# Kernel optimization log

Measured on AMD Instinct MI355X. Metric: run time of the kernel, lower is better.

Reference implementation:

```python
import jax, jax.numpy as jnp
from jax import lax
import numpy as np

DIM = 512      # latent channel dim
K = 1024       # codebook size
KS = 320       # conv kernel size (== stride -> non-overlapping frames)
STRIDE = 320
B, L = 16, 160000  # 10s of 16kHz audio


def setup_inputs() -> dict:
    key = jax.random.key(0)
    ks = jax.random.split(key, 8)
    wav = jax.random.normal(ks[0], (B, 1, L), jnp.float32)
    enc_w = jax.random.normal(ks[1], (DIM, 1, KS), jnp.float32) * 0.05
    enc_b = jnp.zeros((DIM,), jnp.float32)
    codebook = jax.random.normal(ks[2], (K, DIM), jnp.float32)
    lin_w = jax.random.normal(ks[3], (DIM, DIM), jnp.float32) * 0.02
    lin_b = jnp.zeros((DIM,), jnp.float32)
    film_w = jax.random.normal(ks[4], (2 * DIM, DIM), jnp.float32) * 0.02
    film_b = jnp.zeros((2 * DIM,), jnp.float32)
    dec_w = jax.random.normal(ks[5], (DIM, 1, KS), jnp.float32) * 0.05
    dec_b = jnp.zeros((1,), jnp.float32)
    return dict(wav=wav, enc_w=enc_w, enc_b=enc_b, codebook=codebook,
                lin_w=lin_w, lin_b=lin_b, film_w=film_w, film_b=film_b,
                dec_w=dec_w, dec_b=dec_b)


def reference(wav, enc_w, enc_b, codebook, lin_w, lin_b, film_w, film_b, dec_w, dec_b):
    # --- NAC encoder: strided Conv1d, wav [B,1,L] -> emb [B,D,T] ---
    emb = lax.conv_general_dilated(
        wav, enc_w, window_strides=(STRIDE,), padding='VALID',
        dimension_numbers=('NCH', 'OIH', 'NCH')) + enc_b[None, :, None]

    # --- time-averaged embedding for conditioning ---
    time_avg = emb.mean(axis=-1)  # [B, D]

    # --- VQ encode: nearest codebook entry per frame ---
    x = emb.transpose(0, 2, 1)  # [B, T, D]
    # squared L2 distances [B, T, K]
    dist = (x * x).sum(-1, keepdims=True) \
         - 2.0 * jnp.einsum('btd,kd->btk', x, codebook) \
         + (codebook * codebook).sum(-1)
    codes = jnp.argmin(dist, axis=-1)  # [B, T] int

    # --- VQ decode: codebook gather ---
    emb_r = codebook[codes].transpose(0, 2, 1)  # [B, D, T]

    # --- linear on pooled embedding ---
    cond = time_avg @ lin_w.T + lin_b  # [B, D]

    # --- FiLM modulation: gamma * x + beta per channel ---
    gb = cond @ film_w.T + film_b      # [B, 2D]
    gamma, beta = jnp.split(gb, 2, axis=-1)
    modulated = gamma[:, :, None] * emb_r + beta[:, :, None]  # [B, D, T]

    # --- NAC decoder: transposed Conv1d back to waveform [B,1,L] ---
    out = lax.conv_transpose(
        modulated, dec_w, strides=(STRIDE,), padding='VALID',
        dimension_numbers=('NCH', 'IOH', 'NCH')) + dec_b[None, :, None]
    return out
```

## Files before the change

kernel.cpp:

```cpp
#include <hip/hip_runtime.h>

#define FR   8000
#define FRP  8192
#define DD   512
#define CK   1024
#define KSZ  320
#define TT   500
#define NB   16

typedef unsigned int u32;
typedef unsigned short u16;
typedef __attribute__((ext_vector_type(8))) short b8;
typedef __attribute__((ext_vector_type(4))) float f4;

__device__ __forceinline__ float bf2f(u16 h) {
    u32 u = ((u32)h) << 16;
    return __builtin_bit_cast(float, u);
}
__device__ __forceinline__ u16 f2bf(float f) {
    u32 u = __builtin_bit_cast(u32, f);
    u32 r = u + 0x7FFFu + ((u >> 16) & 1u);
    return (u16)(r >> 16);
}

__device__ __forceinline__ void gld16(const u16* g, u16* s) {
    __builtin_amdgcn_global_load_lds(
        (const __attribute__((address_space(1))) u32*)g,
        (__attribute__((address_space(3))) u32*)s, 16, 0, 0);
}

__device__ __forceinline__ f4 mfma(b8 a, b8 b, f4 c) {
    return __builtin_amdgcn_mfma_f32_16x16x32_bf16(a, b, c, 0, 0, 0);
}

__device__ __forceinline__ void split8(float4 a, float4 b, u16* dh, u16* dl) {
    float xs[8] = {a.x, a.y, a.z, a.w, b.x, b.y, b.z, b.w};
    union { u16 u[8]; b8 v; } H, L;
#pragma unroll
    for (int i = 0; i < 8; ++i) {
        u16 h = f2bf(xs[i]);
        H.u[i] = h;
        L.u[i] = f2bf(xs[i] - bf2f(h));
    }
    *(b8*)dh = H.v;
    *(b8*)dl = L.v;
}

__global__ __launch_bounds__(256) void k_prep(const float* __restrict__ enc_w,
                                              u16* __restrict__ ewh, u16* __restrict__ ewl,
                                              const float* __restrict__ cb,
                                              u16* __restrict__ cbh, u16* __restrict__ cbl,
                                              const float* __restrict__ dw,
                                              u16* __restrict__ dwfh, u16* __restrict__ dwfl,
                                              float* __restrict__ cbn,
                                              float* __restrict__ tsum) {
    const int bid = blockIdx.x, tid = threadIdx.x;
    if (bid < 80) {
        int i = (bid * 256 + tid) * 8;
        float4 a = *(const float4*)&enc_w[i];
        float4 b = *(const float4*)&enc_w[i + 4];
        split8(a, b, &ewh[i], &ewl[i]);
    } else if (bid < 336) {
        int i = ((bid - 80) * 256 + tid) * 8;
        float4 a = *(const float4*)&cb[i];
        float4 b = *(const float4*)&cb[i + 4];
        split8(a, b, &cbh[i], &cbl[i]);
    } else if (bid < 368) {
        int c = (bid - 336) * 32 + (tid >> 3);
        int l = tid & 7;
        float s = 0.f;
        for (int j = l * 4; j < DD; j += 32) {
            float4 v = *(const float4*)&cb[c * DD + j];
            s += v.x * v.x + v.y * v.y + v.z * v.z + v.w * v.w;
        }
        s += __shfl_xor(s, 1);
        s += __shfl_xor(s, 2);
        s += __shfl_xor(s, 4);
        if (l == 0) cbn[c] = s;
    } else if (bid < 416) {
        int bid2 = bid - 368;
        int d0 = (bid2 & 7) * 64;
        int sb = bid2 >> 3;
        int s0 = sb * 64;
        if (sb == 5) {
            b8 z = {};
#pragma unroll
            for (int k = 0; k < 2; ++k) {
                int lin = tid * 2 + k;
                int row = 320 + (lin >> 3);
                int col = (lin & 7) * 8;
                *(b8*)&dwfh[(size_t)row * DD + d0 + col] = z;
                *(b8*)&dwfl[(size_t)row * DD + d0 + col] = z;
            }
            return;
        }
        __shared__ float t64[64][68];
        const int u0 = 256 - s0;
#pragma unroll
        for (int p = 0; p < 4; ++p) {
            int row = (tid >> 4) + 16 * p;
            int c4 = (tid & 15) * 4;
            float4 v = *(const float4*)&dw[(size_t)(d0 + row) * KSZ + u0 + c4];
            t64[row][c4] = v.x; t64[row][c4 + 1] = v.y;
            t64[row][c4 + 2] = v.z; t64[row][c4 + 3] = v.w;
        }
        __syncthreads();
        const int i = tid >> 2;
        const int jq = (tid & 3) * 16;
        union { u16 u[8]; b8 v; } H0, L0, H1, L1;
#pragma unroll
        for (int j = 0; j < 8; ++j) {
            float m = t64[jq + j][63 - i];
            u16 h = f2bf(m);
            H0.u[j] = h; L0.u[j] = f2bf(m - bf2f(h));
            float m2 = t64[jq + 8 + j][63 - i];
            u16 h2 = f2bf(m2);
            H1.u[j] = h2; L1.u[j] = f2bf(m2 - bf2f(h2));
        }
        size_t o = (size_t)(s0 + i) * DD + d0 + jq;
        *(b8*)&dwfh[o] = H0.v; *(b8*)&dwfh[o + 8] = H1.v;
        *(b8*)&dwfl[o] = L0.v; *(b8*)&dwfl[o + 8] = L1.v;
    } else {
        float4 z = {0.f, 0.f, 0.f, 0.f};
#pragma unroll
        for (int k = 0; k < 8; ++k)
            *(float4*)&tsum[(tid * 8 + k) * 4] = z;
    }
}

#define PIPELINE(NT, STRIDE)                                                  \
    stg(0, 0);                                                                \
    stg(1, STRIDE);                                                           \
    int cur = 0;                                                              \
    for (int t = 0; t < NT; ++t) {                                            \
        if (t < NT - 1) asm volatile("s_waitcnt vmcnt(8)" ::: "memory");      \
        else            asm volatile("s_waitcnt vmcnt(0)" ::: "memory");      \
        __builtin_amdgcn_s_barrier();                                         \
        asm volatile("" ::: "memory");                                        \
        compute(cur);                                                         \
        asm volatile("" ::: "memory");                                        \
        __builtin_amdgcn_s_barrier();                                         \
        if (t < NT - 2) stg(cur, (t + 2) * STRIDE);                           \
        cur ^= 1;                                                             \
    }

struct AW { float4 x0, x1, y0, y1; };

__global__ __launch_bounds__(256, 2) void k_enc(const float* __restrict__ wav,
                                                const u16* __restrict__ Bhg,
                                                const u16* __restrict__ Blg,
                                                const float* __restrict__ eb,
                                                u16* __restrict__ embh,
                                                u16* __restrict__ embl,
                                                float* __restrict__ tsum) {
    __shared__ __align__(16) u16 Ah[2][4096], Al[2][4096], Bh[2][4096], Bl[2][4096];
    __shared__ float tred[2][128][2];
    const int tid = threadIdx.x;
    const int l = tid & 63, w = tid >> 6, wm = w >> 1, wn = w & 1;
    const int lane16 = l & 15, laneK = l >> 4;
    const int g = blockIdx.x;
    const int xcd = g & 7, slot = g >> 3;
    const int f0 = (xcd * 8 + (slot & 7)) * 128;
    const int d0 = (slot >> 3) * 128;

    const int p0 = w * 128 + l, p1 = p0 + 64;
    const int r0 = p0 >> 2, q0 = (p0 & 3) ^ ((r0 >> 1) & 3);
    const int r1 = p1 >> 2, q1 = (p1 & 3) ^ ((r1 >> 1) & 3);
    const u16* gB0h = Bhg + (size_t)(d0 + r0) * KSZ + q0 * 8;
    const u16* gB1h = Bhg + (size_t)(d0 + r1) * KSZ + q1 * 8;
    const u16* gB0l = Blg + (size_t)(d0 + r0) * KSZ + q0 * 8;
    const u16* gB1l = Blg + (size_t)(d0 + r1) * KSZ + q1 * 8;

    const int pa0 = tid, pa1 = tid + 256;
    const int ra0 = pa0 >> 2, qa0 = (pa0 & 3) ^ ((ra0 >> 1) & 3);
    const int ra1 = pa1 >> 2, qa1 = (pa1 & 3) ^ ((ra1 >> 1) & 3);
    int fa0 = f0 + ra0; if (fa0 > FR - 1) fa0 = FR - 1;
    int fa1 = f0 + ra1; if (fa1 > FR - 1) fa1 = FR - 1;
    const float* wv0 = wav + (size_t)fa0 * KSZ + qa0 * 8;
    const float* wv1 = wav + (size_t)fa1 * KSZ + qa1 * 8;

    int offA[4], offB[4];
#pragma unroll
    for (int i = 0; i < 4; ++i) {
        int ra = wm * 64 + i * 16 + lane16;
        offA[i] = (ra * 4 + (laneK ^ ((ra >> 1) & 3))) * 8;
        int rb = wn * 64 + i * 16 + lane16;
        offB[i] = (rb * 4 + (laneK ^ ((rb >> 1) & 3))) * 8;
    }

    f4 zero = {0.f, 0.f, 0.f, 0.f};
    f4 acc[4][4];
#pragma unroll
    for (int i = 0; i < 4; ++i)
#pragma unroll
        for (int j = 0; j < 4; ++j) acc[i][j] = zero;

    auto loadA = [&](int kt) {
        AW v;
        v.x0 = *(const float4*)(wv0 + kt);
        v.x1 = *(const float4*)(wv0 + kt + 4);
        v.y0 = *(const float4*)(wv1 + kt);
        v.y1 = *(const float4*)(wv1 + kt + 4);
        return v;
    };
    auto writeA = [&](int buf, const AW& v) {
        split8(v.x0, v.x1, Ah[buf] + pa0 * 8, Al[buf] + pa0 * 8);
        split8(v.y0, v.y1, Ah[buf] + pa1 * 8, Al[buf] + pa1 * 8);
    };
    auto stgB = [&](int buf, int kt) {
        gld16(gB0h + kt, Bh[buf] + w * 1024);
        gld16(gB1h + kt, Bh[buf] + w * 1024 + 512);
        gld16(gB0l + kt, Bl[buf] + w * 1024);
        gld16(gB1l + kt, Bl[buf] + w * 1024 + 512);
    };
    auto compute = [&](int buf) {
        b8 ah[4], al[4], bh[4], bl[4];
#pragma unroll
        for (int i = 0; i < 4; ++i) {
            ah[i] = *(const b8*)(Ah[buf] + offA[i]);
            al[i] = *(const b8*)(Al[buf] + offA[i]);
            bh[i] = *(const b8*)(Bh[buf] + offB[i]);
            bl[i] = *(const b8*)(Bl[buf] + offB[i]);
        }
#pragma unroll
        for (int mi = 0; mi < 4; ++mi)
#pragma unroll
            for (int ni = 0; ni < 4; ++ni) {
                acc[mi][ni] = mfma(ah[mi], bh[ni], acc[mi][ni]);
                acc[mi][ni] = mfma(ah[mi], bl[ni], acc[mi][ni]);
                acc[mi][ni] = mfma(al[mi], bh[ni], acc[mi][ni]);
            }
    };

    {
        AW v0 = loadA(0);
        AW v1 = loadA(32);
        stgB(0, 0);
        stgB(1, 32);
        writeA(0, v0);
        writeA(1, v1);
    }
    int cur = 0;
    for (int t = 0; t < 10; ++t) {
        if (t < 9) asm volatile("s_waitcnt vmcnt(4) lgkmcnt(0)" ::: "memory");
        else       asm volatile("s_waitcnt vmcnt(0) lgkmcnt(0)" ::: "memory");
        __builtin_amdgcn_s_barrier();
        asm volatile("" ::: "memory");
        compute(cur);
        asm volatile("" ::: "memory");
        __builtin_amdgcn_s_barrier();
        if (t < 8) {
            AW v = loadA((t + 2) * 32);
            stgB(cur, (t + 2) * 32);
            writeA(cur, v);
        }
        cur ^= 1;
    }

    float ebv[4];
#pragma unroll
    for (int ni = 0; ni < 4; ++ni) ebv[ni] = eb[d0 + wn * 64 + ni * 16 + lane16];

    const int bA = f0 / TT;
    const int fB = min((bA + 1) * TT, f0 + 128);
    float sumA[4] = {}, sumB[4] = {};
#pragma unroll
    for (int mi = 0; mi < 4; ++mi)
#pragma unroll
        for (int q = 0; q < 4; ++q) {
            int f = f0 + wm * 64 + mi * 16 + laneK * 4 + q;
            bool live = f < FR;
            bool sideA = f < fB;
#pragma unroll
            for (int ni = 0; ni < 4; ++ni) {
                int d = d0 + wn * 64 + ni * 16 + lane16;
                float v = acc[mi][ni][q] + ebv[ni];
                u16 h = f2bf(v);
                size_t o = (size_t)f * DD + d;
                embh[o] = h;
                embl[o] = f2bf(v - bf2f(h));
                if (live) { if (sideA) sumA[ni] += v; else sumB[ni] += v; }
            }
        }
#pragma unroll
    for (int m = 16; m <= 32; m <<= 1)
#pragma unroll
        for (int ni = 0; ni < 4; ++ni) {
            sumA[ni] += __shfl_xor(sumA[ni], m);
            sumB[ni] += __shfl_xor(sumB[ni], m);
        }
    if (laneK == 0)
#pragma unroll
        for (int ni = 0; ni < 4; ++ni) {
            tred[wm][wn * 64 + ni * 16 + lane16][0] = sumA[ni];
            tred[wm][wn * 64 + ni * 16 + lane16][1] = sumB[ni];
        }
    __syncthreads();
    if (tid < 128 && bA < NB) {
        float a = tred[0][tid][0] + tred[1][tid][0];
        int d = d0 + tid;
        atomicAdd(&tsum[bA * DD + d], a);
        if (fB < f0 + 128 && bA + 1 < NB) {
            float b = tred[0][tid][1] + tred[1][tid][1];
            atomicAdd(&tsum[(bA + 1) * DD + d], b);
        }
    }
}

__global__ __launch_bounds__(256) void k_cond(const float* __restrict__ tsum,
                                              const float* __restrict__ lw,
                                              const float* __restrict__ lb,
                                              float* __restrict__ cond) {
    __shared__ float stv[NB * DD];
    const float inv = 1.0f / TT;
    for (int i = threadIdx.x * 4; i < NB * DD; i += 1024) {
        float4 v = *(const float4*)&tsum[i];
        v.x *= inv; v.y *= inv; v.z *= inv; v.w *= inv;
        *(float4*)&stv[i] = v;
    }
    __syncthreads();
    const int w = threadIdx.x >> 6, lane = threadIdx.x & 63;
    const int row = blockIdx.x * 4 + w;
    float wv[8];
#pragma unroll
    for (int j = 0; j < 8; ++j) wv[j] = lw[(size_t)row * DD + lane + 64 * j];
    float r[NB];
#pragma unroll
    for (int b = 0; b < NB; ++b) {
        float s = 0.f;
#pragma unroll
        for (int j = 0; j < 8; ++j) s += wv[j] * stv[b * DD + lane + 64 * j];
        r[b] = s;
    }
#pragma unroll
    for (int m = 32; m >= 1; m >>= 1)
#pragma unroll
        for (int b = 0; b < NB; ++b) r[b] += __shfl_xor(r[b], m);
    if (lane < NB) cond[lane * DD + row] = r[lane] + lb[row];
}

__global__ __launch_bounds__(256) void k_film(const float* __restrict__ cond,
                                              const float* __restrict__ fw,
                                              const float* __restrict__ fb,
                                              float* __restrict__ gbv) {
    __shared__ float sc[NB * DD];
    for (int i = threadIdx.x * 4; i < NB * DD; i += 1024)
        *(float4*)&sc[i] = *(const float4*)&cond[i];
    __syncthreads();
    const int w = threadIdx.x >> 6, lane = threadIdx.x & 63;
    const int row = blockIdx.x * 4 + w;
    float wv[8];
#pragma unroll
    for (int j = 0; j < 8; ++j) wv[j] = fw[(size_t)row * DD + lane + 64 * j];
    float r[NB];
#pragma unroll
    for (int b = 0; b < NB; ++b) {
        float s = 0.f;
#pragma unroll
        for (int j = 0; j < 8; ++j) s += wv[j] * sc[b * DD + lane + 64 * j];
        r[b] = s;
    }
#pragma unroll
    for (int m = 32; m >= 1; m >>= 1)
#pragma unroll
        for (int b = 0; b < NB; ++b) r[b] += __shfl_xor(r[b], m);
    if (lane < NB) gbv[lane * 2 * DD + row] = r[lane] + fb[row];
}

__global__ __launch_bounds__(256, 2) void k_dist(const u16* __restrict__ Ahg,
                                                 const u16* __restrict__ Alg,
                                                 const u16* __restrict__ Bhg,
                                                 const u16* __restrict__ Blg,
                                                 const float* __restrict__ cbn,
                                                 float* __restrict__ pmin,
                                                 int* __restrict__ pidx) {
    __shared__ __align__(16) u16 Ah[2][4096], Al[2][4096], Bh[2][4096], Bl[2][4096];
    __shared__ float s_best[128][2];
    __shared__ int s_bidx[128][2];
    const int tid = threadIdx.x;
    const int l = tid & 63, w = tid >> 6, wm = w >> 1, wn = w & 1;
    const int lane16 = l & 15, laneK = l >> 4;
    const int g = blockIdx.x;
    const int xcd = g & 7, slot = g >> 3;
    const int f0 = (xcd * 8 + (slot & 7)) * 128;
    const int cy = slot >> 3;
    const int c0 = cy * 128;

    const int p0 = w * 128 + l, p1 = p0 + 64;
    const int r0 = p0 >> 2, q0 = (p0 & 3) ^ ((r0 >> 1) & 3);
    const int r1 = p1 >> 2, q1 = (p1 & 3) ^ ((r1 >> 1) & 3);
    const u16* gA0h = Ahg + (size_t)(f0 + r0) * DD + q0 * 8;
    const u16* gA1h = Ahg + (size_t)(f0 + r1) * DD + q1 * 8;
    const u16* gA0l = Alg + (size_t)(f0 + r0) * DD + q0 * 8;
    const u16* gA1l = Alg + (size_t)(f0 + r1) * DD + q1 * 8;
    const u16* gB0h = Bhg + (size_t)(c0 + r0) * DD + q0 * 8;
    const u16* gB1h = Bhg + (size_t)(c0 + r1) * DD + q1 * 8;
    const u16* gB0l = Blg + (size_t)(c0 + r0) * DD + q0 * 8;
    const u16* gB1l = Blg + (size_t)(c0 + r1) * DD + q1 * 8;

    int offA[4], offB[4];
#pragma unroll
    for (int i = 0; i < 4; ++i) {
        int ra = wm * 64 + i * 16 + lane16;
        offA[i] = (ra * 4 + (laneK ^ ((ra >> 1) & 3))) * 8;
        int rb = wn * 64 + i * 16 + lane16;
        offB[i] = (rb * 4 + (laneK ^ ((rb >> 1) & 3))) * 8;
    }

    f4 zero = {0.f, 0.f, 0.f, 0.f};
    f4 acc[4][4];
#pragma unroll
    for (int i = 0; i < 4; ++i)
#pragma unroll
        for (int j = 0; j < 4; ++j) acc[i][j] = zero;

    auto stg = [&](int buf, int kt) {
        gld16(gA0h + kt, Ah[buf] + w * 1024);
        gld16(gA1h + kt, Ah[buf] + w * 1024 + 512);
        gld16(gA0l + kt, Al[buf] + w * 1024);
        gld16(gA1l + kt, Al[buf] + w * 1024 + 512);
        gld16(gB0h + kt, Bh[buf] + w * 1024);
        gld16(gB1h + kt, Bh[buf] + w * 1024 + 512);
        gld16(gB0l + kt, Bl[buf] + w * 1024);
        gld16(gB1l + kt, Bl[buf] + w * 1024 + 512);
    };
    auto compute = [&](int buf) {
        b8 ah[4], al[4], bh[4], bl[4];
#pragma unroll
        for (int i = 0; i < 4; ++i) {
            ah[i] = *(const b8*)(Ah[buf] + offA[i]);
            al[i] = *(const b8*)(Al[buf] + offA[i]);
            bh[i] = *(const b8*)(Bh[buf] + offB[i]);
            bl[i] = *(const b8*)(Bl[buf] + offB[i]);
        }
#pragma unroll
        for (int mi = 0; mi < 4; ++mi)
#pragma unroll
            for (int ni = 0; ni < 4; ++ni) {
                acc[mi][ni] = mfma(ah[mi], bh[ni], acc[mi][ni]);
                acc[mi][ni] = mfma(ah[mi], bl[ni], acc[mi][ni]);
                acc[mi][ni] = mfma(al[mi], bh[ni], acc[mi][ni]);
            }
    };

    PIPELINE(16, 32)

    float cbv[4];
    int cidx[4];
#pragma unroll
    for (int ni = 0; ni < 4; ++ni) {
        cidx[ni] = c0 + wn * 64 + ni * 16 + lane16;
        cbv[ni] = cbn[cidx[ni]];
    }
#pragma unroll
    for (int mi = 0; mi < 4; ++mi)
#pragma unroll
        for (int q = 0; q < 4; ++q) {
            float best = 3.4e38f;
            int bi = 0x7fffffff;
#pragma unroll
            for (int ni = 0; ni < 4; ++ni) {
                float s = cbv[ni] - 2.0f * acc[mi][ni][q];
                if (s < best || (s == best && cidx[ni] < bi)) { best = s; bi = cidx[ni]; }
            }
#pragma unroll
            for (int m = 8; m >= 1; m >>= 1) {
                float os = __shfl_xor(best, m);
                int oi = __shfl_xor(bi, m);
                if (os < best || (os == best && oi < bi)) { best = os; bi = oi; }
            }
            if (lane16 == 0) {
                int rl = wm * 64 + mi * 16 + laneK * 4 + q;
                s_best[rl][wn] = best;
                s_bidx[rl][wn] = bi;
            }
        }
    __syncthreads();
    if (tid < 128) {
        float b0 = s_best[tid][0], b1 = s_best[tid][1];
        int i0 = s_bidx[tid][0], i1 = s_bidx[tid][1];
        bool t1 = (b1 < b0) || (b1 == b0 && i1 < i0);
        int f = f0 + tid;
        if (f < FR) {
            pmin[f * 8 + cy] = t1 ? b1 : b0;
            pidx[f * 8 + cy] = t1 ? i1 : i0;
        }
    }
}

struct AV {
    float4 c00, c01, g00, g01, e00, e01;
    float4 c10, c11, g10, g11, e10, e11;
};

__global__ __launch_bounds__(256, 2) void k_dec(const float* __restrict__ pmin,
                                                const int* __restrict__ pidx,
                                                const float* __restrict__ cb,
                                                const float* __restrict__ gbv,
                                                const u16* __restrict__ Bhg,
                                                const u16* __restrict__ Blg,
                                                const float* __restrict__ db,
                                                float* __restrict__ out) {
    __shared__ __align__(16) u16 Ah[2][4096], Al[2][4096], Bh[2][4096], Bl[2][4096];
    __shared__ int codes_lds[128];
    __shared__ int b_lds[128];
    const int tid = threadIdx.x;
    const int l = tid & 63, w = tid >> 6, wm = w >> 1, wn = w & 1;
    const int lane16 = l & 15, laneK = l >> 4;
    const int f0 = blockIdx.y * 128, s0 = blockIdx.x * 128;

    if (tid < 128) {
        int f = f0 + tid;
        int fc = (f < FR) ? f : FR - 1;
        float best = pmin[fc * 8];
        int bi = pidx[fc * 8];
#pragma unroll
        for (int y = 1; y < 8; ++y) {
            float s = pmin[fc * 8 + y];
            if (s < best) { best = s; bi = pidx[fc * 8 + y]; }
        }
        codes_lds[tid] = bi;
        b_lds[tid] = fc / TT;
    }
    __syncthreads();

    const int p0 = w * 128 + l, p1 = p0 + 64;
    const int r0 = p0 >> 2, q0 = (p0 & 3) ^ ((r0 >> 1) & 3);
    const int r1 = p1 >> 2, q1 = (p1 & 3) ^ ((r1 >> 1) & 3);
    const u16* gB0h = Bhg + (size_t)(s0 + r0) * DD + q0 * 8;
    const u16* gB1h = Bhg + (size_t)(s0 + r1) * DD + q1 * 8;
    const u16* gB0l = Blg + (size_t)(s0 + r0) * DD + q0 * 8;
    const u16* gB1l = Blg + (size_t)(s0 + r1) * DD + q1 * 8;

    const int pa0 = tid, pa1 = tid + 256;
    const int ra0 = pa0 >> 2, qa0 = (pa0 & 3) ^ ((ra0 >> 1) & 3);
    const int ra1 = pa1 >> 2, qa1 = (pa1 & 3) ^ ((ra1 >> 1) & 3);
    const float* cp0 = cb + (size_t)codes_lds[ra0] * DD + qa0 * 8;
    const float* cp1 = cb + (size_t)codes_lds[ra1] * DD + qa1 * 8;
    const float* gp0 = gbv + b_lds[ra0] * 2 * DD + qa0 * 8;
    const float* gp1 = gbv + b_lds[ra1] * 2 * DD + qa1 * 8;

    int offA[4], offB[4];
#pragma unroll
    for (int i = 0; i < 4; ++i) {
        int ra = wm * 64 + i * 16 + lane16;
        offA[i] = (ra * 4 + (laneK ^ ((ra >> 1) & 3))) * 8;
        int rb = wn * 64 + i * 16 + lane16;
        offB[i] = (rb * 4 + (laneK ^ ((rb >> 1) & 3))) * 8;
    }

    f4 zero = {0.f, 0.f, 0.f, 0.f};
    f4 acc[4][4];
#pragma unroll
    for (int i = 0; i < 4; ++i)
#pragma unroll
        for (int j = 0; j < 4; ++j) acc[i][j] = zero;

    auto stgB = [&](int buf, int kt) {
        gld16(gB0h + kt, Bh[buf] + w * 1024);
        gld16(gB1h + kt, Bh[buf] + w * 1024 + 512);
        gld16(gB0l + kt, Bl[buf] + w * 1024);
        gld16(gB1l + kt, Bl[buf] + w * 1024 + 512);
    };
    auto loadA = [&](int kt) {
        AV v;
        v.c00 = *(const float4*)(cp0 + kt);
        v.c01 = *(const float4*)(cp0 + kt + 4);
        v.g00 = *(const float4*)(gp0 + kt);
        v.g01 = *(const float4*)(gp0 + kt + 4);
        v.e00 = *(const float4*)(gp0 + DD + kt);
        v.e01 = *(const float4*)(gp0 + DD + kt + 4);
        v.c10 = *(const float4*)(cp1 + kt);
        v.c11 = *(const float4*)(cp1 + kt + 4);
        v.g10 = *(const float4*)(gp1 + kt);
        v.g11 = *(const float4*)(gp1 + kt + 4);
        v.e10 = *(const float4*)(gp1 + DD + kt);
        v.e11 = *(const float4*)(gp1 + DD + kt + 4);
        return v;
    };
    auto writeA = [&](int buf, const AV& v) {
        float4 m00, m01, m10, m11;
        m00.x = v.g00.x * v.c00.x + v.e00.x; m00.y = v.g00.y * v.c00.y + v.e00.y;
        m00.z = v.g00.z * v.c00.z + v.e00.z; m00.w = v.g00.w * v.c00.w + v.e00.w;
        m01.x = v.g01.x * v.c01.x + v.e01.x; m01.y = v.g01.y * v.c01.y + v.e01.y;
        m01.z = v.g01.z * v.c01.z + v.e01.z; m01.w = v.g01.w * v.c01.w + v.e01.w;
        m10.x = v.g10.x * v.c10.x + v.e10.x; m10.y = v.g10.y * v.c10.y + v.e10.y;
        m10.z = v.g10.z * v.c10.z + v.e10.z; m10.w = v.g10.w * v.c10.w + v.e10.w;
        m11.x = v.g11.x * v.c11.x + v.e11.x; m11.y = v.g11.y * v.c11.y + v.e11.y;
        m11.z = v.g11.z * v.c11.z + v.e11.z; m11.w = v.g11.w * v.c11.w + v.e11.w;
        split8(m00, m01, Ah[buf] + pa0 * 8, Al[buf] + pa0 * 8);
        split8(m10, m11, Ah[buf] + pa1 * 8, Al[buf] + pa1 * 8);
    };
    auto compute = [&](int buf) {
        b8 ah[4], al[4], bh[4], bl[4];
#pragma unroll
        for (int i = 0; i < 4; ++i) {
            ah[i] = *(const b8*)(Ah[buf] + offA[i]);
            al[i] = *(const b8*)(Al[buf] + offA[i]);
            bh[i] = *(const b8*)(Bh[buf] + offB[i]);
            bl[i] = *(const b8*)(Bl[buf] + offB[i]);
        }
#pragma unroll
        for (int mi = 0; mi < 4; ++mi)
#pragma unroll
            for (int ni = 0; ni < 4; ++ni) {
                acc[mi][ni] = mfma(ah[mi], bh[ni], acc[mi][ni]);
                acc[mi][ni] = mfma(ah[mi], bl[ni], acc[mi][ni]);
                acc[mi][ni] = mfma(al[mi], bh[ni], acc[mi][ni]);
            }
    };

    {
        AV v0 = loadA(0);
        AV v1 = loadA(32);
        stgB(0, 0);
        stgB(1, 32);
        writeA(0, v0);
        writeA(1, v1);
    }
    int cur = 0;
    for (int t = 0; t < 16; ++t) {
        if (t < 15) asm volatile("s_waitcnt vmcnt(4) lgkmcnt(0)" ::: "memory");
        else        asm volatile("s_waitcnt vmcnt(0) lgkmcnt(0)" ::: "memory");
        __builtin_amdgcn_s_barrier();
        asm volatile("" ::: "memory");
        compute(cur);
        asm volatile("" ::: "memory");
        __builtin_amdgcn_s_barrier();
        if (t < 14) {
            AV v = loadA((t + 2) * 32);
            stgB(cur, (t + 2) * 32);
            writeA(cur, v);
        }
        cur ^= 1;
    }

    const float d0v = db[0];
#pragma unroll
    for (int mi = 0; mi < 4; ++mi)
#pragma unroll
        for (int q = 0; q < 4; ++q) {
            int f = f0 + wm * 64 + mi * 16 + laneK * 4 + q;
            if (f < FR) {
#pragma unroll
                for (int ni = 0; ni < 4; ++ni) {
                    int s = s0 + wn * 64 + ni * 16 + lane16;
                    if (s < KSZ) out[(size_t)f * KSZ + s] = acc[mi][ni][q] + d0v;
                }
            }
        }
}

extern "C" void kernel_launch(void* const* d_in, const int* in_sizes, int n_in,
                              void* d_out, int out_size, void* d_ws, size_t ws_size,
                              hipStream_t stream) {
    const float* wav    = (const float*)d_in[0];
    const float* enc_w  = (const float*)d_in[1];
    const float* enc_b  = (const float*)d_in[2];
    const float* cb     = (const float*)d_in[3];
    const float* lin_w  = (const float*)d_in[4];
    const float* lin_b  = (const float*)d_in[5];
    const float* film_w = (const float*)d_in[6];
    const float* film_b = (const float*)d_in[7];
    const float* dec_w  = (const float*)d_in[8];
    const float* dec_b  = (const float*)d_in[9];
    float* out = (float*)d_out;

    char* p = (char*)d_ws;
    u16* embh = (u16*)p;                 p += (size_t)FRP * DD * 2;
    u16* embl = (u16*)p;                 p += (size_t)FRP * DD * 2;
    u16* ewh  = (u16*)p;                 p += (size_t)DD * KSZ * 2;
    u16* ewl  = (u16*)p;                 p += (size_t)DD * KSZ * 2;
    u16* cbh  = (u16*)p;                 p += (size_t)CK * DD * 2;
    u16* cbl  = (u16*)p;                 p += (size_t)CK * DD * 2;
    u16* dwfh = (u16*)p;                 p += (size_t)384 * DD * 2;
    u16* dwfl = (u16*)p;                 p += (size_t)384 * DD * 2;
    float* cbn  = (float*)p;             p += CK * 4;
    float* tsum = (float*)p;             p += NB * DD * 4;
    float* cond = (float*)p;             p += NB * DD * 4;
    float* gbv  = (float*)p;             p += NB * 2 * DD * 4;
    float* pmin = (float*)p;             p += FR * 8 * 4;
    int*   pidx = (int*)p;               p += FR * 8 * 4;

    k_prep<<<dim3(417), 256, 0, stream>>>(enc_w, ewh, ewl, cb, cbh, cbl,
                                          dec_w, dwfh, dwfl, cbn, tsum);
    k_enc<<<dim3(256), 256, 0, stream>>>(wav, ewh, ewl, enc_b, embh, embl, tsum);
    k_cond<<<dim3(128), 256, 0, stream>>>(tsum, lin_w, lin_b, cond);
    k_film<<<dim3(256), 256, 0, stream>>>(cond, film_w, film_b, gbv);
    k_dist<<<dim3(512), 256, 0, stream>>>(embh, embl, cbh, cbl, cbn, pmin, pidx);
    k_dec<<<dim3(3, 63), 256, 0, stream>>>(pmin, pidx, cb, gbv, dwfh, dwfl, dec_b, out);
}
```

Baseline: 172.2 us.

## Use 512-thread blocks for enc/dist, smaller 64x64 tiles for dec, MFMA priority

k_enc and k_dist now run with 8 waves per 128x128 tile, each wave owning a 64x32 sub-tile, so every thread stages fewer global loads and holds fewer accumulators. k_dec moves to 64x64 tiles on a 5x125 grid that exactly covers the 8000x320 output, which removes the bounds checks and padded waste. s_setprio raises wave priority around the MFMA bursts, and k_dist is launched before the small cond/film kernels. The aim is more resident waves to hide latency and better CU utilisation, paid for with more LDS fragment reloads per MFMA and a 4-way cross-wave argmin reduction.

```diff
diff --git a/kernel.cpp b/kernel.cpp
--- a/kernel.cpp
+++ b/kernel.cpp
@@ -128,25 +128,7 @@
     }
 }
 
-#define PIPELINE(NT, STRIDE)                                                  \
-    stg(0, 0);                                                                \
-    stg(1, STRIDE);                                                           \
-    int cur = 0;                                                              \
-    for (int t = 0; t < NT; ++t) {                                            \
-        if (t < NT - 1) asm volatile("s_waitcnt vmcnt(8)" ::: "memory");      \
-        else            asm volatile("s_waitcnt vmcnt(0)" ::: "memory");      \
-        __builtin_amdgcn_s_barrier();                                         \
-        asm volatile("" ::: "memory");                                        \
-        compute(cur);                                                         \
-        asm volatile("" ::: "memory");                                        \
-        __builtin_amdgcn_s_barrier();                                         \
-        if (t < NT - 2) stg(cur, (t + 2) * STRIDE);                           \
-        cur ^= 1;                                                             \
-    }
-
-struct AW { float4 x0, x1, y0, y1; };
-
-__global__ __launch_bounds__(256, 2) void k_enc(const float* __restrict__ wav,
+__global__ __launch_bounds__(512, 4) void k_enc(const float* __restrict__ wav,
                                                 const u16* __restrict__ Bhg,
                                                 const u16* __restrict__ Blg,
                                                 const float* __restrict__ eb,
@@ -156,80 +138,75 @@
     __shared__ __align__(16) u16 Ah[2][4096], Al[2][4096], Bh[2][4096], Bl[2][4096];
     __shared__ float tred[2][128][2];
     const int tid = threadIdx.x;
-    const int l = tid & 63, w = tid >> 6, wm = w >> 1, wn = w & 1;
+    const int l = tid & 63, w = tid >> 6, wm = w >> 2, wn = w & 3;
     const int lane16 = l & 15, laneK = l >> 4;
     const int g = blockIdx.x;
     const int xcd = g & 7, slot = g >> 3;
     const int f0 = (xcd * 8 + (slot & 7)) * 128;
     const int d0 = (slot >> 3) * 128;
 
-    const int p0 = w * 128 + l, p1 = p0 + 64;
-    const int r0 = p0 >> 2, q0 = (p0 & 3) ^ ((r0 >> 1) & 3);
-    const int r1 = p1 >> 2, q1 = (p1 & 3) ^ ((r1 >> 1) & 3);
-    const u16* gB0h = Bhg + (size_t)(d0 + r0) * KSZ + q0 * 8;
-    const u16* gB1h = Bhg + (size_t)(d0 + r1) * KSZ + q1 * 8;
-    const u16* gB0l = Blg + (size_t)(d0 + r0) * KSZ + q0 * 8;
-    const u16* gB1l = Blg + (size_t)(d0 + r1) * KSZ + q1 * 8;
-
-    const int pa0 = tid, pa1 = tid + 256;
-    const int ra0 = pa0 >> 2, qa0 = (pa0 & 3) ^ ((ra0 >> 1) & 3);
-    const int ra1 = pa1 >> 2, qa1 = (pa1 & 3) ^ ((ra1 >> 1) & 3);
-    int fa0 = f0 + ra0; if (fa0 > FR - 1) fa0 = FR - 1;
-    int fa1 = f0 + ra1; if (fa1 > FR - 1) fa1 = FR - 1;
-    const float* wv0 = wav + (size_t)fa0 * KSZ + qa0 * 8;
-    const float* wv1 = wav + (size_t)fa1 * KSZ + qa1 * 8;
-
-    int offA[4], offB[4];
+    const int sr = tid >> 2;
+    const int sq = (tid & 3) ^ ((sr >> 1) & 3);
+    int fa = f0 + sr; if (fa > FR - 1) fa = FR - 1;
+    const float* wv = wav + (size_t)fa * KSZ + sq * 8;
+    const u16* gBh = Bhg + (size_t)(d0 + sr) * KSZ + sq * 8;
+    const u16* gBl = Blg + (size_t)(d0 + sr) * KSZ + sq * 8;
+
+    int offA[4], offB[2];
 #pragma unroll
     for (int i = 0; i < 4; ++i) {
         int ra = wm * 64 + i * 16 + lane16;
         offA[i] = (ra * 4 + (laneK ^ ((ra >> 1) & 3))) * 8;
-        int rb = wn * 64 + i * 16 + lane16;
+    }
+#pragma unroll
+    for (int i = 0; i < 2; ++i) {
+        int rb = wn * 32 + i * 16 + lane16;
         offB[i] = (rb * 4 + (laneK ^ ((rb >> 1) & 3))) * 8;
     }
 
     f4 zero = {0.f, 0.f, 0.f, 0.f};
-    f4 acc[4][4];
+    f4 acc[4][2];
 #pragma unroll
     for (int i = 0; i < 4; ++i)
 #pragma unroll
-        for (int j = 0; j < 4; ++j) acc[i][j] = zero;
-
+        for (int j = 0; j < 2; ++j) acc[i][j] = zero;
+
+    struct AW { float4 x0, x1; };
     auto loadA = [&](int kt) {
         AW v;
-        v.x0 = *(const float4*)(wv0 + kt);
-        v.x1 = *(const float4*)(wv0 + kt + 4);
-        v.y0 = *(const float4*)(wv1 + kt);
-        v.y1 = *(const float4*)(wv1 + kt + 4);
+        v.x0 = *(const float4*)(wv + kt);
+        v.x1 = *(const float4*)(wv + kt + 4);
         return v;
     };
     auto writeA = [&](int buf, const AW& v) {
-        split8(v.x0, v.x1, Ah[buf] + pa0 * 8, Al[buf] + pa0 * 8);
-        split8(v.y0, v.y1, Ah[buf] + pa1 * 8, Al[buf] + pa1 * 8);
+        split8(v.x0, v.x1, Ah[buf] + tid * 8, Al[buf] + tid * 8);
     };
     auto stgB = [&](int buf, int kt) {
-        gld16(gB0h + kt, Bh[buf] + w * 1024);
-        gld16(gB1h + kt, Bh[buf] + w * 1024 + 512);
-        gld16(gB0l + kt, Bl[buf] + w * 1024);
-        gld16(gB1l + kt, Bl[buf] + w * 1024 + 512);
+        gld16(gBh + kt, Bh[buf] + w * 512);
+        gld16(gBl + kt, Bl[buf] + w * 512);
     };
     auto compute = [&](int buf) {
-        b8 ah[4], al[4], bh[4], bl[4];
+        b8 ah[4], al[4], bh[2], bl[2];
 #pragma unroll
         for (int i = 0; i < 4; ++i) {
             ah[i] = *(const b8*)(Ah[buf] + offA[i]);
             al[i] = *(const b8*)(Al[buf] + offA[i]);
+        }
+#pragma unroll
+        for (int i = 0; i < 2; ++i) {
             bh[i] = *(const b8*)(Bh[buf] + offB[i]);
             bl[i] = *(const b8*)(Bl[buf] + offB[i]);
         }
+        __builtin_amdgcn_s_setprio(1);
 #pragma unroll
         for (int mi = 0; mi < 4; ++mi)
 #pragma unroll
-            for (int ni = 0; ni < 4; ++ni) {
+            for (int ni = 0; ni < 2; ++ni) {
                 acc[mi][ni] = mfma(ah[mi], bh[ni], acc[mi][ni]);
                 acc[mi][ni] = mfma(ah[mi], bl[ni], acc[mi][ni]);
                 acc[mi][ni] = mfma(al[mi], bh[ni], acc[mi][ni]);
             }
+        __builtin_amdgcn_s_setprio(0);
     };
 
     {
@@ -242,7 +219,7 @@
     }
     int cur = 0;
     for (int t = 0; t < 10; ++t) {
-        if (t < 9) asm volatile("s_waitcnt vmcnt(4) lgkmcnt(0)" ::: "memory");
+        if (t < 9) asm volatile("s_waitcnt vmcnt(2) lgkmcnt(0)" ::: "memory");
         else       asm volatile("s_waitcnt vmcnt(0) lgkmcnt(0)" ::: "memory");
         __builtin_amdgcn_s_barrier();
         asm volatile("" ::: "memory");
@@ -257,13 +234,13 @@
         cur ^= 1;
     }
 
-    float ebv[4];
-#pragma unroll
-    for (int ni = 0; ni < 4; ++ni) ebv[ni] = eb[d0 + wn * 64 + ni * 16 + lane16];
+    float ebv[2];
+#pragma unroll
+    for (int ni = 0; ni < 2; ++ni) ebv[ni] = eb[d0 + wn * 32 + ni * 16 + lane16];
 
     const int bA = f0 / TT;
     const int fB = min((bA + 1) * TT, f0 + 128);
-    float sumA[4] = {}, sumB[4] = {};
+    float sumA[2] = {}, sumB[2] = {};
 #pragma unroll
     for (int mi = 0; mi < 4; ++mi)
 #pragma unroll
@@ -272,8 +249,8 @@
             bool live = f < FR;
             bool sideA = f < fB;
 #pragma unroll
-            for (int ni = 0; ni < 4; ++ni) {
-                int d = d0 + wn * 64 + ni * 16 + lane16;
+            for (int ni = 0; ni < 2; ++ni) {
+                int d = d0 + wn * 32 + ni * 16 + lane16;
                 float v = acc[mi][ni][q] + ebv[ni];
                 u16 h = f2bf(v);
                 size_t o = (size_t)f * DD + d;
@@ -285,15 +262,15 @@
 #pragma unroll
     for (int m = 16; m <= 32; m <<= 1)
 #pragma unroll
-        for (int ni = 0; ni < 4; ++ni) {
+        for (int ni = 0; ni < 2; ++ni) {
             sumA[ni] += __shfl_xor(sumA[ni], m);
             sumB[ni] += __shfl_xor(sumB[ni], m);
         }
     if (laneK == 0)
 #pragma unroll
-        for (int ni = 0; ni < 4; ++ni) {
-            tred[wm][wn * 64 + ni * 16 + lane16][0] = sumA[ni];
-            tred[wm][wn * 64 + ni * 16 + lane16][1] = sumB[ni];
+        for (int ni = 0; ni < 2; ++ni) {
+            tred[wm][wn * 32 + ni * 16 + lane16][0] = sumA[ni];
+            tred[wm][wn * 32 + ni * 16 + lane16][1] = sumB[ni];
         }
     __syncthreads();
     if (tid < 128 && bA < NB) {
@@ -367,7 +344,7 @@
     if (lane < NB) gbv[lane * 2 * DD + row] = r[lane] + fb[row];
 }
 
-__global__ __launch_bounds__(256, 2) void k_dist(const u16* __restrict__ Ahg,
+__global__ __launch_bounds__(512, 4) void k_dist(const u16* __restrict__ Ahg,
                                                  const u16* __restrict__ Alg,
                                                  const u16* __restrict__ Bhg,
                                                  const u16* __restrict__ Blg,
@@ -375,81 +352,93 @@
                                                  float* __restrict__ pmin,
                                                  int* __restrict__ pidx) {
     __shared__ __align__(16) u16 Ah[2][4096], Al[2][4096], Bh[2][4096], Bl[2][4096];
-    __shared__ float s_best[128][2];
-    __shared__ int s_bidx[128][2];
+    __shared__ float s_best[128][4];
+    __shared__ int s_bidx[128][4];
     const int tid = threadIdx.x;
-    const int l = tid & 63, w = tid >> 6, wm = w >> 1, wn = w & 1;
+    const int l = tid & 63, w = tid >> 6, wm = w >> 2, wn = w & 3;
     const int lane16 = l & 15, laneK = l >> 4;
     const int g = blockIdx.x;
     const int xcd = g & 7, slot = g >> 3;
-    const int f0 = (xcd * 8 + (slot & 7)) * 128;
+    const int fbase = (xcd * 8 + (slot & 7)) * 128;
     const int cy = slot >> 3;
     const int c0 = cy * 128;
 
-    const int p0 = w * 128 + l, p1 = p0 + 64;
-    const int r0 = p0 >> 2, q0 = (p0 & 3) ^ ((r0 >> 1) & 3);
-    const int r1 = p1 >> 2, q1 = (p1 & 3) ^ ((r1 >> 1) & 3);
-    const u16* gA0h = Ahg + (size_t)(f0 + r0) * DD + q0 * 8;
-    const u16* gA1h = Ahg + (size_t)(f0 + r1) * DD + q1 * 8;
-    const u16* gA0l = Alg + (size_t)(f0 + r0) * DD + q0 * 8;
-    const u16* gA1l = Alg + (size_t)(f0 + r1) * DD + q1 * 8;
-    const u16* gB0h = Bhg + (size_t)(c0 + r0) * DD + q0 * 8;
-    const u16* gB1h = Bhg + (size_t)(c0 + r1) * DD + q1 * 8;
-    const u16* gB0l = Blg + (size_t)(c0 + r0) * DD + q0 * 8;
-    const u16* gB1l = Blg + (size_t)(c0 + r1) * DD + q1 * 8;
-
-    int offA[4], offB[4];
+    const int sr = tid >> 2;
+    const int sq = (tid & 3) ^ ((sr >> 1) & 3);
+    const u16* gAh = Ahg + (size_t)(fbase + sr) * DD + sq * 8;
+    const u16* gAl = Alg + (size_t)(fbase + sr) * DD + sq * 8;
+    const u16* gBh = Bhg + (size_t)(c0 + sr) * DD + sq * 8;
+    const u16* gBl = Blg + (size_t)(c0 + sr) * DD + sq * 8;
+
+    int offA[4], offB[2];
 #pragma unroll
     for (int i = 0; i < 4; ++i) {
         int ra = wm * 64 + i * 16 + lane16;
         offA[i] = (ra * 4 + (laneK ^ ((ra >> 1) & 3))) * 8;
-        int rb = wn * 64 + i * 16 + lane16;
+    }
+#pragma unroll
+    for (int i = 0; i < 2; ++i) {
+        int rb = wn * 32 + i * 16 + lane16;
         offB[i] = (rb * 4 + (laneK ^ ((rb >> 1) & 3))) * 8;
     }
 
     f4 zero = {0.f, 0.f, 0.f, 0.f};
-    f4 acc[4][4];
+    f4 acc[4][2];
 #pragma unroll
     for (int i = 0; i < 4; ++i)
 #pragma unroll
-        for (int j = 0; j < 4; ++j) acc[i][j] = zero;
+        for (int j = 0; j < 2; ++j) acc[i][j] = zero;
 
     auto stg = [&](int buf, int kt) {
-        gld16(gA0h + kt, Ah[buf] + w * 1024);
-        gld16(gA1h + kt, Ah[buf] + w * 1024 + 512);
-        gld16(gA0l + kt, Al[buf] + w * 1024);
-        gld16(gA1l + kt, Al[buf] + w * 1024 + 512);
-        gld16(gB0h + kt, Bh[buf] + w * 1024);
-        gld16(gB1h + kt, Bh[buf] + w * 1024 + 512);
-        gld16(gB0l + kt, Bl[buf] + w * 1024);
-        gld16(gB1l + kt, Bl[buf] + w * 1024 + 512);
+        gld16(gAh + kt, Ah[buf] + w * 512);
+        gld16(gAl + kt, Al[buf] + w * 512);
+        gld16(gBh + kt, Bh[buf] + w * 512);
+        gld16(gBl + kt, Bl[buf] + w * 512);
     };
     auto compute = [&](int buf) {
-        b8 ah[4], al[4], bh[4], bl[4];
+        b8 ah[4], al[4], bh[2], bl[2];
 #pragma unroll
         for (int i = 0; i < 4; ++i) {
             ah[i] = *(const b8*)(Ah[buf] + offA[i]);
             al[i] = *(const b8*)(Al[buf] + offA[i]);
+        }
+#pragma unroll
+        for (int i = 0; i < 2; ++i) {
             bh[i] = *(const b8*)(Bh[buf] + offB[i]);
             bl[i] = *(const b8*)(Bl[buf] + offB[i]);
         }
+        __builtin_amdgcn_s_setprio(1);
 #pragma unroll
         for (int mi = 0; mi < 4; ++mi)
 #pragma unroll
-            for (int ni = 0; ni < 4; ++ni) {
+            for (int ni = 0; ni < 2; ++ni) {
                 acc[mi][ni] = mfma(ah[mi], bh[ni], acc[mi][ni]);
                 acc[mi][ni] = mfma(ah[mi], bl[ni], acc[mi][ni]);
                 acc[mi][ni] = mfma(al[mi], bh[ni], acc[mi][ni]);
             }
-    };
-
-    PIPELINE(16, 32)
-
-    float cbv[4];
-    int cidx[4];
-#pragma unroll
-    for (int ni = 0; ni < 4; ++ni) {
-        cidx[ni] = c0 + wn * 64 + ni * 16 + lane16;
+        __builtin_amdgcn_s_setprio(0);
+    };
+
+    stg(0, 0);
+    stg(1, 32);
+    int cur = 0;
+    for (int t = 0; t < 16; ++t) {
+        if (t < 15) asm volatile("s_waitcnt vmcnt(4)" ::: "memory");
+        else        asm volatile("s_waitcnt vmcnt(0)" ::: "memory");
+        __builtin_amdgcn_s_barrier();
+        asm volatile("" ::: "memory");
+        compute(cur);
+        asm volatile("" ::: "memory");
+        __builtin_amdgcn_s_barrier();
+        if (t < 14) stg(cur, (t + 2) * 32);
+        cur ^= 1;
+    }
+
+    float cbv[2];
+    int cidx[2];
+#pragma unroll
+    for (int ni = 0; ni < 2; ++ni) {
+        cidx[ni] = c0 + wn * 32 + ni * 16 + lane16;
         cbv[ni] = cbn[cidx[ni]];
     }
 #pragma unroll
@@ -459,7 +448,7 @@
             float best = 3.4e38f;
             int bi = 0x7fffffff;
 #pragma unroll
-            for (int ni = 0; ni < 4; ++ni) {
+            for (int ni = 0; ni < 2; ++ni) {
                 float s = cbv[ni] - 2.0f * acc[mi][ni][q];
                 if (s < best || (s == best && cidx[ni] < bi)) { best = s; bi = cidx[ni]; }
             }
@@ -477,23 +466,23 @@
         }
     __syncthreads();
     if (tid < 128) {
-        float b0 = s_best[tid][0], b1 = s_best[tid][1];
-        int i0 = s_bidx[tid][0], i1 = s_bidx[tid][1];
-        bool t1 = (b1 < b0) || (b1 == b0 && i1 < i0);
-        int f = f0 + tid;
+        float best = s_best[tid][0];
+        int bi = s_bidx[tid][0];
+#pragma unroll
+        for (int y = 1; y < 4; ++y) {
+            float s = s_best[tid][y];
+            int ii = s_bidx[tid][y];
+            if (s < best || (s == best && ii < bi)) { best = s; bi = ii; }
+        }
+        int f = fbase + tid;
         if (f < FR) {
-            pmin[f * 8 + cy] = t1 ? b1 : b0;
-            pidx[f * 8 + cy] = t1 ? i1 : i0;
-        }
-    }
-}
-
-struct AV {
-    float4 c00, c01, g00, g01, e00, e01;
-    float4 c10, c11, g10, g11, e10, e11;
-};
-
-__global__ __launch_bounds__(256, 2) void k_dec(const float* __restrict__ pmin,
+            pmin[f * 8 + cy] = best;
+            pidx[f * 8 + cy] = bi;
+        }
+    }
+}
+
+__global__ __launch_bounds__(256, 4) void k_dec(const float* __restrict__ pmin,
                                                 const int* __restrict__ pidx,
                                                 const float* __restrict__ cb,
                                                 const float* __restrict__ gbv,
@@ -501,17 +490,16 @@
                                                 const u16* __restrict__ Blg,
                                                 const float* __restrict__ db,
                                                 float* __restrict__ out) {
-    __shared__ __align__(16) u16 Ah[2][4096], Al[2][4096], Bh[2][4096], Bl[2][4096];
-    __shared__ int codes_lds[128];
-    __shared__ int b_lds[128];
+    __shared__ __align__(16) u16 Ah[2][2048], Al[2][2048], Bh[2][2048], Bl[2][2048];
+    __shared__ int codes_lds[64];
+    __shared__ int b_lds[64];
     const int tid = threadIdx.x;
     const int l = tid & 63, w = tid >> 6, wm = w >> 1, wn = w & 1;
     const int lane16 = l & 15, laneK = l >> 4;
-    const int f0 = blockIdx.y * 128, s0 = blockIdx.x * 128;
-
-    if (tid < 128) {
-        int f = f0 + tid;
-        int fc = (f < FR) ? f : FR - 1;
+    const int f0 = blockIdx.y * 64, s0 = blockIdx.x * 64;
+
+    if (tid < 64) {
+        int fc = f0 + tid;
         float best = pmin[fc * 8];
         int bi = pidx[fc * 8];
 #pragma unroll
@@ -524,90 +512,72 @@
     }
     __syncthreads();
 
-    const int p0 = w * 128 + l, p1 = p0 + 64;
-    const int r0 = p0 >> 2, q0 = (p0 & 3) ^ ((r0 >> 1) & 3);
-    const int r1 = p1 >> 2, q1 = (p1 & 3) ^ ((r1 >> 1) & 3);
-    const u16* gB0h = Bhg + (size_t)(s0 + r0) * DD + q0 * 8;
-    const u16* gB1h = Bhg + (size_t)(s0 + r1) * DD + q1 * 8;
-    const u16* gB0l = Blg + (size_t)(s0 + r0) * DD + q0 * 8;
-    const u16* gB1l = Blg + (size_t)(s0 + r1) * DD + q1 * 8;
-
-    const int pa0 = tid, pa1 = tid + 256;
-    const int ra0 = pa0 >> 2, qa0 = (pa0 & 3) ^ ((ra0 >> 1) & 3);
-    const int ra1 = pa1 >> 2, qa1 = (pa1 & 3) ^ ((ra1 >> 1) & 3);
-    const float* cp0 = cb + (size_t)codes_lds[ra0] * DD + qa0 * 8;
-    const float* cp1 = cb + (size_t)codes_lds[ra1] * DD + qa1 * 8;
-    const float* gp0 = gbv + b_lds[ra0] * 2 * DD + qa0 * 8;
-    const float* gp1 = gbv + b_lds[ra1] * 2 * DD + qa1 * 8;
-
-    int offA[4], offB[4];
-#pragma unroll
-    for (int i = 0; i < 4; ++i) {
-        int ra = wm * 64 + i * 16 + lane16;
+    const int sr = tid >> 2;
+    const int sq = (tid & 3) ^ ((sr >> 1) & 3);
+    const float* cp = cb + (size_t)codes_lds[sr] * DD + sq * 8;
+    const float* gp = gbv + b_lds[sr] * 2 * DD + sq * 8;
+    const float* ep = gp + DD;
+    const u16* gBh = Bhg + (size_t)(s0 + sr) * DD + sq * 8;
+    const u16* gBl = Blg + (size_t)(s0 + sr) * DD + sq * 8;
+
+    int offA[2], offB[2];
+#pragma unroll
+    for (int i = 0; i < 2; ++i) {
+        int ra = wm * 32 + i * 16 + lane16;
         offA[i] = (ra * 4 + (laneK ^ ((ra >> 1) & 3))) * 8;
-        int rb = wn * 64 + i * 16 + lane16;
+        int rb = wn * 32 + i * 16 + lane16;
         offB[i] = (rb * 4 + (laneK ^ ((rb >> 1) & 3))) * 8;
     }
 
     f4 zero = {0.f, 0.f, 0.f, 0.f};
-    f4 acc[4][4];
-#pragma unroll
-    for (int i = 0; i < 4; ++i)
-#pragma unroll
-        for (int j = 0; j < 4; ++j) acc[i][j] = zero;
-
-    auto stgB = [&](int buf, int kt) {
-        gld16(gB0h + kt, Bh[buf] + w * 1024);
-        gld16(gB1h + kt, Bh[buf] + w * 1024 + 512);
-        gld16(gB0l + kt, Bl[buf] + w * 1024);
-        gld16(gB1l + kt, Bl[buf] + w * 1024 + 512);
-    };
+    f4 acc[2][2];
+#pragma unroll
+    for (int i = 0; i < 2; ++i)
+#pragma unroll
+        for (int j = 0; j < 2; ++j) acc[i][j] = zero;
+
+    struct AV { float4 c0, c1, g0, g1, e0, e1; };
     auto loadA = [&](int kt) {
         AV v;
-        v.c00 = *(const float4*)(cp0 + kt);
-        v.c01 = *(const float4*)(cp0 + kt + 4);
-        v.g00 = *(const float4*)(gp0 + kt);
-        v.g01 = *(const float4*)(gp0 + kt + 4);
-        v.e00 = *(const float4*)(gp0 + DD + kt);
-        v.e01 = *(const float4*)(gp0 + DD + kt + 4);
-        v.c10 = *(const float4*)(cp1 + kt);
-        v.c11 = *(const float4*)(cp1 + kt + 4);
-        v.g10 = *(const float4*)(gp1 + kt);
-        v.g11 = *(const float4*)(gp1 + kt + 4);
-        v.e10 = *(const float4*)(gp1 + DD + kt);
-        v.e11 = *(const float4*)(gp1 + DD + kt + 4);
+        v.c0 = *(const float4*)(cp + kt);
+        v.c1 = *(const float4*)(cp + kt + 4);
+        v.g0 = *(const float4*)(gp + kt);
+        v.g1 = *(const float4*)(gp + kt + 4);
+        v.e0 = *(const float4*)(ep + kt);
+        v.e1 = *(const float4*)(ep + kt + 4);
         return v;
     };
     auto writeA = [&](int buf, const AV& v) {
-        float4 m00, m01, m10, m11;
-        m00.x = v.g00.x * v.c00.x + v.e00.x; m00.y = v.g00.y * v.c00.y + v.e00.y;
-        m00.z = v.g00.z * v.c00.z + v.e00.z; m00.w = v.g00.w * v.c00.w + v.e00.w;
-        m01.x = v.g01.x * v.c01.x + v.e01.x; m01.y = v.g01.y * v.c01.y + v.e01.y;
-        m01.z = v.g01.z * v.c01.z + v.e01.z; m01.w = v.g01.w * v.c01.w + v.e01.w;
-        m10.x = v.g10.x * v.c10.x + v.e10.x; m10.y = v.g10.y * v.c10.y + v.e10.y;
-        m10.z = v.g10.z * v.c10.z + v.e10.z; m10.w = v.g10.w * v.c10.w + v.e10.w;
-        m11.x = v.g11.x * v.c11.x + v.e11.x; m11.y = v.g11.y * v.c11.y + v.e11.y;
-        m11.z = v.g11.z * v.c11.z + v.e11.z; m11.w = v.g11.w * v.c11.w + v.e11.w;
-        split8(m00, m01, Ah[buf] + pa0 * 8, Al[buf] + pa0 * 8);
-        split8(m10, m11, Ah[buf] + pa1 * 8, Al[buf] + pa1 * 8);
+        float4 m0, m1;
+        m0.x = v.g0.x * v.c0.x + v.e0.x; m0.y = v.g0.y * v.c0.y + v.e0.y;
+        m0.z = v.g0.z * v.c0.z + v.e0.z; m0.w = v.g0.w * v.c0.w + v.e0.w;
+        m1.x = v.g1.x * v.c1.x + v.e1.x; m1.y = v.g1.y * v.c1.y + v.e1.y;
+        m1.z = v.g1.z * v.c1.z + v.e1.z; m1.w = v.g1.w * v.c1.w + v.e1.w;
+        split8(m0, m1, Ah[buf] + tid * 8, Al[buf] + tid * 8);
+    };
+    auto stgB = [&](int buf, int kt) {
+        gld16(gBh + kt, Bh[buf] + w * 512);
+        gld16(gBl + kt, Bl[buf] + w * 512);
     };
     auto compute = [&](int buf) {
-        b8 ah[4], al[4], bh[4], bl[4];
-#pragma unroll
-        for (int i = 0; i < 4; ++i) {
+        b8 ah[2], al[2], bh[2], bl[2];
+#pragma unroll
+        for (int i = 0; i < 2; ++i) {
             ah[i] = *(const b8*)(Ah[buf] + offA[i]);
             al[i] = *(const b8*)(Al[buf] + offA[i]);
             bh[i] = *(const b8*)(Bh[buf] + offB[i]);
             bl[i] = *(const b8*)(Bl[buf] + offB[i]);
         }
-#pragma unroll
-        for (int mi = 0; mi < 4; ++mi)
-#pragma unroll
-            for (int ni = 0; ni < 4; ++ni) {
+        __builtin_amdgcn_s_setprio(1);
+#pragma unroll
+        for (int mi = 0; mi < 2; ++mi)
+#pragma unroll
+            for (int ni = 0; ni < 2; ++ni) {
                 acc[mi][ni] = mfma(ah[mi], bh[ni], acc[mi][ni]);
                 acc[mi][ni] = mfma(ah[mi], bl[ni], acc[mi][ni]);
                 acc[mi][ni] = mfma(al[mi], bh[ni], acc[mi][ni]);
             }
+        __builtin_amdgcn_s_setprio(0);
     };
 
     {
@@ -620,7 +590,7 @@
     }
     int cur = 0;
     for (int t = 0; t < 16; ++t) {
-        if (t < 15) asm volatile("s_waitcnt vmcnt(4) lgkmcnt(0)" ::: "memory");
+        if (t < 15) asm volatile("s_waitcnt vmcnt(2) lgkmcnt(0)" ::: "memory");
         else        asm volatile("s_waitcnt vmcnt(0) lgkmcnt(0)" ::: "memory");
         __builtin_amdgcn_s_barrier();
         asm volatile("" ::: "memory");
@@ -637,16 +607,14 @@
 
     const float d0v = db[0];
 #pragma unroll
-    for (int mi = 0; mi < 4; ++mi)
+    for (int mi = 0; mi < 2; ++mi)
 #pragma unroll
         for (int q = 0; q < 4; ++q) {
-            int f = f0 + wm * 64 + mi * 16 + laneK * 4 + q;
-            if (f < FR) {
-#pragma unroll
-                for (int ni = 0; ni < 4; ++ni) {
-                    int s = s0 + wn * 64 + ni * 16 + lane16;
-                    if (s < KSZ) out[(size_t)f * KSZ + s] = acc[mi][ni][q] + d0v;
-                }
+            int f = f0 + wm * 32 + mi * 16 + laneK * 4 + q;
+#pragma unroll
+            for (int ni = 0; ni < 2; ++ni) {
+                int s = s0 + wn * 32 + ni * 16 + lane16;
+                out[(size_t)f * KSZ + s] = acc[mi][ni][q] + d0v;
             }
         }
 }
@@ -684,9 +652,9 @@
 
     k_prep<<<dim3(417), 256, 0, stream>>>(enc_w, ewh, ewl, cb, cbh, cbl,
                                           dec_w, dwfh, dwfl, cbn, tsum);
-    k_enc<<<dim3(256), 256, 0, stream>>>(wav, ewh, ewl, enc_b, embh, embl, tsum);
+    k_enc<<<dim3(256), 512, 0, stream>>>(wav, ewh, ewl, enc_b, embh, embl, tsum);
+    k_dist<<<dim3(512), 512, 0, stream>>>(embh, embl, cbh, cbl, cbn, pmin, pidx);
     k_cond<<<dim3(128), 256, 0, stream>>>(tsum, lin_w, lin_b, cond);
     k_film<<<dim3(256), 256, 0, stream>>>(cond, film_w, film_b, gbv);
-    k_dist<<<dim3(512), 256, 0, stream>>>(embh, embl, cbh, cbl, cbn, pmin, pidx);
-    k_dec<<<dim3(3, 63), 256, 0, stream>>>(pmin, pidx, cb, gbv, dwfh, dwfl, dec_b, out);
-}
+    k_dec<<<dim3(5, 125), 256, 0, stream>>>(pmin, pidx, cb, gbv, dwfh, dwfl, dec_b, out);
+}
```

Result: faster. 166.7 us (-3.2%).
